# Performance work log

Hardware: AMD Instinct MI355X
Metric: run time of the kernel (lower is better)

## Reference

```python
import jax, jax.numpy as jnp
import numpy as np

N, S, C, K, V = 8, 8192, 1, 1024, 64  # batch, samples, n_channels, n_classes, vec_len


def setup_inputs() -> dict:
    key = jax.random.key(0)
    k1, k2 = jax.random.split(key)
    x0 = jax.random.normal(k1, (N, S, C, V), dtype=jnp.float32)
    embedding0 = jax.random.normal(k2, (C, K, V), dtype=jnp.float32) * 0.001
    return {"x0": x0, "embedding0": embedding0}


def reference(x0, embedding0):
    # normalize=False path of the original module
    x = x0
    emb = embedding0
    Ns = x.shape[0] * x.shape[1]
    xf = x.reshape(Ns, C, V)  # (Ns, C, V)
    # squared distances ||x - e||^2 without materializing (Ns, C, K, V)
    d2 = (
        jnp.sum(xf * xf, axis=-1)[:, :, None]
        - 2.0 * jnp.einsum("ncv,ckv->nck", xf, emb)
        + jnp.sum(emb * emb, axis=-1)[None, :, :]
    )
    index = jnp.argmin(d2, axis=2)  # (Ns, C); argmin of dist == argmin of dist^2
    # histogram entropy (matches torch histc over bins 0..K-1, divided by len(index)=Ns)
    counts = jnp.zeros((K,), jnp.float32).at[index.reshape(-1)].add(1.0)
    prob = counts / Ns
    safe_log = jnp.log(jnp.where(counts > 0, prob, 1.0))
    entropy = -jnp.sum(jnp.where(counts > 0, prob * safe_log, 0.0))
    # gather codewords: embedding[c, index[n,c]]
    output = emb[jnp.arange(C)[None, :], index].reshape(x.shape)
    out0 = jax.lax.stop_gradient(output - x) + x  # straight-through
    out1 = jnp.sum((jax.lax.stop_gradient(x) - output) ** 2, axis=-1)  # (N,S,C)
    out2 = jnp.sum((x - jax.lax.stop_gradient(output)) ** 2, axis=-1)  # (N,S,C)
    return (out0, out1, out2, entropy)
```

## Files before the change

### kernel.cpp

```cpp
#include <hip/hip_runtime.h>
#include <math.h>

#define NS   65536
#define KK   1024
#define VV   64
#define SPB  256
#define NB   (NS / SPB)
#define CBB  131072

#define OUT0_OFF 0
#define OUT1_OFF 4194304
#define OUT2_OFF 4259840
#define ENT_OFF  4325376


typedef __attribute__((ext_vector_type(8))) short bf16x8;
typedef __attribute__((ext_vector_type(4))) float f32x4;

#define ASYNC16(gp, lp) __builtin_amdgcn_global_load_lds(                      \
    (const __attribute__((address_space(1))) unsigned int*)(gp),               \
    (__attribute__((address_space(3))) unsigned int*)(lp), 16, 0, 0)

__device__ __forceinline__ short f2bf(float f) {
    unsigned u = __float_as_uint(f);
    u = (u + 0x7fffu + ((u >> 16) & 1u)) >> 16;
    return (short)u;
}

__global__ void vq_prep(const float* __restrict__ emb, unsigned int* __restrict__ hist,
                        float* __restrict__ cinit, short* __restrict__ cb,
                        unsigned int* __restrict__ entCnt) {
    int t = blockIdx.x * blockDim.x + threadIdx.x;
    if (t == 0) entCnt[0] = 0u;
    if (t < KK) {
        hist[t] = 0u;
        const float4* e4 = (const float4*)(emb + (size_t)t * VV);
        const int ch = t >> 8, cw = t & 255;
        short* base = cb + (size_t)ch * (256 * VV) + cw * 64;
        float s = 0.f;
        union { short sh[8]; bf16x8 v; } pk;
        #pragma unroll
        for (int g = 0; g < 8; ++g) {
            float4 f0 = e4[2 * g], f1 = e4[2 * g + 1];
            s = fmaf(f0.x, f0.x, s); s = fmaf(f0.y, f0.y, s);
            s = fmaf(f0.z, f0.z, s); s = fmaf(f0.w, f0.w, s);
            s = fmaf(f1.x, f1.x, s); s = fmaf(f1.y, f1.y, s);
            s = fmaf(f1.z, f1.z, s); s = fmaf(f1.w, f1.w, s);
            pk.sh[0] = f2bf(f0.x); pk.sh[1] = f2bf(f0.y);
            pk.sh[2] = f2bf(f0.z); pk.sh[3] = f2bf(f0.w);
            pk.sh[4] = f2bf(f1.x); pk.sh[5] = f2bf(f1.y);
            pk.sh[6] = f2bf(f1.z); pk.sh[7] = f2bf(f1.w);
            *(bf16x8*)(base + ((g ^ (cw & 7)) * 8)) = pk.v;
        }
        cinit[t] = 1.0f - 0.5f * s;
    }
}

__global__ __launch_bounds__(1024, 4) void vq_main(
    const float* __restrict__ x, const float* __restrict__ emb,
    const float* __restrict__ cinit, const short* __restrict__ cb,
    unsigned int* __restrict__ hist,
    float* __restrict__ out0, float* __restrict__ out1, float* __restrict__ out2,
    float* __restrict__ entOut)
{
    __shared__ __align__(16) char  sCB[CBB];
    __shared__ __align__(16) float sCI[KK];
    __shared__ unsigned sPk2[2][SPB];
    __shared__ float    sXn[SPB];
    __shared__ float    sPart[16];
    __shared__ unsigned sLast;

    const int tid  = threadIdx.x;
    const int lane = tid & 63;
    const int wv   = tid >> 6;
    const int grp  = wv & 7;
    const int kh   = wv >> 3;
    const int col  = lane & 15;
    const int quad = lane >> 4;
    const int samp0 = blockIdx.x * SPB;
    const int wbase = grp * 32;

    {
        const char* g0 = (const char*)cb;
        #pragma unroll
        for (int i = 0; i < 8; ++i) {
            const int off = (i * 1024 + tid) * 16;
            ASYNC16(g0 + off, sCB + off);
        }
        sCI[tid] = cinit[tid];
    }

    bf16x8 a[4];
    float  xn[2];
    #pragma unroll
    for (int mt = 0; mt < 2; ++mt) {
        const float* xp = x + (size_t)(samp0 + wbase + mt * 16 + col) * VV + quad * 8;
        float4 p0 = *(const float4*)(xp);
        float4 p1 = *(const float4*)(xp + 4);
        float4 p2 = *(const float4*)(xp + 32);
        float4 p3 = *(const float4*)(xp + 36);
        bf16x8 lo, hi;
        lo[0]=f2bf(p0.x); lo[1]=f2bf(p0.y); lo[2]=f2bf(p0.z); lo[3]=f2bf(p0.w);
        lo[4]=f2bf(p1.x); lo[5]=f2bf(p1.y); lo[6]=f2bf(p1.z); lo[7]=f2bf(p1.w);
        hi[0]=f2bf(p2.x); hi[1]=f2bf(p2.y); hi[2]=f2bf(p2.z); hi[3]=f2bf(p2.w);
        hi[4]=f2bf(p3.x); hi[5]=f2bf(p3.y); hi[6]=f2bf(p3.z); hi[7]=f2bf(p3.w);
        a[2 * mt] = lo; a[2 * mt + 1] = hi;
        float s = 0.f;
        s=fmaf(p0.x,p0.x,s); s=fmaf(p0.y,p0.y,s); s=fmaf(p0.z,p0.z,s); s=fmaf(p0.w,p0.w,s);
        s=fmaf(p1.x,p1.x,s); s=fmaf(p1.y,p1.y,s); s=fmaf(p1.z,p1.z,s); s=fmaf(p1.w,p1.w,s);
        s=fmaf(p2.x,p2.x,s); s=fmaf(p2.y,p2.y,s); s=fmaf(p2.z,p2.z,s); s=fmaf(p2.w,p2.w,s);
        s=fmaf(p3.x,p3.x,s); s=fmaf(p3.y,p3.y,s); s=fmaf(p3.z,p3.z,s); s=fmaf(p3.w,p3.w,s);
        xn[mt] = s;
    }
    if (kh == 0) {
        #pragma unroll
        for (int mt = 0; mt < 2; ++mt) {
            xn[mt] += __shfl_xor(xn[mt], 16, 64);
            xn[mt] += __shfl_xor(xn[mt], 32, 64);
        }
    }
    __syncthreads();

    unsigned pm[8];
    #pragma unroll
    for (int j = 0; j < 8; ++j) pm[j] = 0u;

    const int rb0off = col * 128 + ((quad ^ (col & 7)) << 4);
    const int rb1off = col * 128 + (((4 + quad) ^ (col & 7)) << 4);
    const unsigned invc = 1023u - (unsigned)(kh * 512) - (unsigned)col;
    const char*  B  = sCB + kh * 65536;
    const float* CI = sCI + kh * 512;

    unsigned pkp[8];
    #pragma unroll 8
    for (int t = 0; t < 32; ++t) {
        bf16x8 b0 = *(const bf16x8*)(B + t * 2048 + rb0off);
        bf16x8 b1 = *(const bf16x8*)(B + t * 2048 + rb1off);
        float ci = CI[t * 16 + col];
        f32x4 cv = {ci, ci, ci, ci};
        const unsigned inv = invc - (unsigned)(t * 16);
        unsigned pk2[8];
        #pragma unroll
        for (int mt = 0; mt < 2; ++mt) {
            f32x4 acc = __builtin_amdgcn_mfma_f32_16x16x32_bf16(a[2*mt],     b0, cv,  0, 0, 0);
            acc       = __builtin_amdgcn_mfma_f32_16x16x32_bf16(a[2*mt + 1], b1, acc, 0, 0, 0);
            #pragma unroll
            for (int r = 0; r < 4; ++r)
                pk2[mt*4+r] = (__float_as_uint(acc[r]) & 0xFFFFFC00u) | inv;
        }
        if (t & 1) {
            #pragma unroll
            for (int j = 0; j < 8; ++j) {
                unsigned t2 = pkp[j] > pk2[j] ? pkp[j] : pk2[j];
                pm[j] = pm[j] > t2 ? pm[j] : t2;
            }
        } else {
            #pragma unroll
            for (int j = 0; j < 8; ++j) pkp[j] = pk2[j];
        }
    }

    #pragma unroll
    for (int off = 1; off < 16; off <<= 1) {
        #pragma unroll
        for (int j = 0; j < 8; ++j) {
            unsigned o = (unsigned)__shfl_xor((int)pm[j], off, 64);
            pm[j] = (o > pm[j]) ? o : pm[j];
        }
    }
    if (col == 0) {
        #pragma unroll
        for (int mt = 0; mt < 2; ++mt)
            #pragma unroll
            for (int r = 0; r < 4; ++r)
                sPk2[kh][wbase + mt * 16 + quad * 4 + r] = pm[mt * 4 + r];
    }
    if (kh == 0 && quad == 0) {
        #pragma unroll
        for (int mt = 0; mt < 2; ++mt) sXn[wbase + mt * 16 + col] = xn[mt];
    }
    __syncthreads();

    if (tid < SPB) {
        unsigned pa = sPk2[0][tid], pb = sPk2[1][tid];
        unsigned p  = pa > pb ? pa : pb;
        sPk2[0][tid] = p;
        int   code = 1023 - (int)(p & 1023u);
        float sf   = __uint_as_float(p & 0xFFFFFC00u);
        float d    = fmaf(-2.f, sf - 1.0f, sXn[tid]);
        int n = samp0 + tid;
        out1[n] = d;
        out2[n] = d;
        atomicAdd(&hist[code], 1u);
    }
    __syncthreads();

    {
        float4* dstB = (float4*)(out0 + (size_t)samp0 * VV);
        #pragma unroll
        for (int i = 0; i < 4; ++i) {
            const int idx  = i * 1024 + tid;
            const int smp  = idx >> 4;
            const int part = idx & 15;
            const int code = 1023 - (int)(sPk2[0][smp] & 1023u);
            dstB[idx] = *((const float4*)(emb + (size_t)code * VV) + part);
        }
    }

    __syncthreads();
    unsigned int* entCnt = (unsigned int*)entOut;
    if (tid == 0)
        sLast = (__hip_atomic_fetch_add(entCnt, 1u, __ATOMIC_ACQ_REL,
                                        __HIP_MEMORY_SCOPE_AGENT) == (NB - 1)) ? 1u : 0u;
    __syncthreads();
    if (sLast) {
        unsigned c = __hip_atomic_load(&hist[tid], __ATOMIC_RELAXED,
                                       __HIP_MEMORY_SCOPE_AGENT);
        float e = 0.f;
        if (c) { float p = (float)c * (1.0f / (float)NS); e = -p * logf(p); }
        #pragma unroll
        for (int off = 32; off > 0; off >>= 1) e += __shfl_down(e, off, 64);
        if (lane == 0) sPart[wv] = e;
        __syncthreads();
        if (tid == 0) {
            float s = 0.f;
            #pragma unroll
            for (int i = 0; i < 16; ++i) s += sPart[i];
            entOut[0] = s;
        }
    }
}

extern "C" void kernel_launch(void* const* d_in, const int* in_sizes, int n_in,
                              void* d_out, int out_size, void* d_ws, size_t ws_size,
                              hipStream_t stream) {
    const float* x   = (const float*)d_in[0];
    const float* emb = (const float*)d_in[1];
    float* out = (float*)d_out;
    unsigned int* hist  = (unsigned int*)d_ws;
    float*        cinit = (float*)((char*)d_ws + 4096);
    short*        cb    = (short*)((char*)d_ws + 8192);

    vq_prep<<<4, 256, 0, stream>>>(emb, hist, cinit, cb, (unsigned int*)(out + ENT_OFF));
    vq_main<<<NB, 1024, 0, stream>>>(x, emb, cinit, cb, hist,
                                     out + OUT0_OFF, out + OUT1_OFF, out + OUT2_OFF,
                                     out + ENT_OFF);
}
```

Measured before the change: 111.3 us.

## Swap operand roles: stage samples in LDS, stream codebook from global into registers

```diff
diff --git a/kernel.cpp b/kernel.cpp
--- a/kernel.cpp
+++ b/kernel.cpp
@@ -4,9 +4,11 @@
 #define NS   65536
 #define KK   1024
 #define VV   64
-#define SPB  256
+#define SPB  128
 #define NB   (NS / SPB)
-#define CBB  131072
+#define NW   8
+#define TPW  4
+#define NPASS 2
 
 #define OUT0_OFF 0
 #define OUT1_OFF 4194304
@@ -16,10 +18,6 @@
 
 typedef __attribute__((ext_vector_type(8))) short bf16x8;
 typedef __attribute__((ext_vector_type(4))) float f32x4;
-
-#define ASYNC16(gp, lp) __builtin_amdgcn_global_load_lds(                      \
-    (const __attribute__((address_space(1))) unsigned int*)(gp),               \
-    (__attribute__((address_space(3))) unsigned int*)(lp), 16, 0, 0)
 
 __device__ __forceinline__ short f2bf(float f) {
     unsigned u = __float_as_uint(f);
@@ -35,8 +33,7 @@
     if (t < KK) {
         hist[t] = 0u;
         const float4* e4 = (const float4*)(emb + (size_t)t * VV);
-        const int ch = t >> 8, cw = t & 255;
-        short* base = cb + (size_t)ch * (256 * VV) + cw * 64;
+        const int T = t >> 4, cc = t & 15;
         float s = 0.f;
         union { short sh[8]; bf16x8 v; } pk;
         #pragma unroll
@@ -50,143 +47,128 @@
             pk.sh[2] = f2bf(f0.z); pk.sh[3] = f2bf(f0.w);
             pk.sh[4] = f2bf(f1.x); pk.sh[5] = f2bf(f1.y);
             pk.sh[6] = f2bf(f1.z); pk.sh[7] = f2bf(f1.w);
-            *(bf16x8*)(base + ((g ^ (cw & 7)) * 8)) = pk.v;
+            short* dst = cb + (size_t)T * 1024 + (g >> 2) * 512 + ((g & 3) * 16 + cc) * 8;
+            *(bf16x8*)dst = pk.v;
         }
         cinit[t] = 1.0f - 0.5f * s;
     }
 }
 
-__global__ __launch_bounds__(1024, 4) void vq_main(
+__global__ __launch_bounds__(512, 4) void vq_main(
     const float* __restrict__ x, const float* __restrict__ emb,
     const float* __restrict__ cinit, const short* __restrict__ cb,
     unsigned int* __restrict__ hist,
     float* __restrict__ out0, float* __restrict__ out1, float* __restrict__ out2,
     float* __restrict__ entOut)
 {
-    __shared__ __align__(16) char  sCB[CBB];
-    __shared__ __align__(16) float sCI[KK];
-    __shared__ unsigned sPk2[2][SPB];
+    __shared__ __align__(16) char  sA[SPB * 128];
     __shared__ float    sXn[SPB];
-    __shared__ float    sPart[16];
+    __shared__ unsigned sRed[SPB][NW + 1];
+    __shared__ unsigned sPkF[SPB];
+    __shared__ float    sPart[NW];
     __shared__ unsigned sLast;
 
     const int tid  = threadIdx.x;
     const int lane = tid & 63;
     const int wv   = tid >> 6;
-    const int grp  = wv & 7;
-    const int kh   = wv >> 3;
     const int col  = lane & 15;
     const int quad = lane >> 4;
     const int samp0 = blockIdx.x * SPB;
-    const int wbase = grp * 32;
 
     {
-        const char* g0 = (const char*)cb;
-        #pragma unroll
-        for (int i = 0; i < 8; ++i) {
-            const int off = (i * 1024 + tid) * 16;
-            ASYNC16(g0 + off, sCB + off);
-        }
-        sCI[tid] = cinit[tid];
-    }
-
-    bf16x8 a[4];
-    float  xn[2];
+        const int s = tid >> 2, q = tid & 3;
+        const float4* xp = (const float4*)(x + (size_t)(samp0 + s) * VV + q * 16);
+        float4 f0 = xp[0], f1 = xp[1], f2 = xp[2], f3 = xp[3];
+        float sm = 0.f;
+        sm=fmaf(f0.x,f0.x,sm); sm=fmaf(f0.y,f0.y,sm); sm=fmaf(f0.z,f0.z,sm); sm=fmaf(f0.w,f0.w,sm);
+        sm=fmaf(f1.x,f1.x,sm); sm=fmaf(f1.y,f1.y,sm); sm=fmaf(f1.z,f1.z,sm); sm=fmaf(f1.w,f1.w,sm);
+        sm=fmaf(f2.x,f2.x,sm); sm=fmaf(f2.y,f2.y,sm); sm=fmaf(f2.z,f2.z,sm); sm=fmaf(f2.w,f2.w,sm);
+        sm=fmaf(f3.x,f3.x,sm); sm=fmaf(f3.y,f3.y,sm); sm=fmaf(f3.z,f3.z,sm); sm=fmaf(f3.w,f3.w,sm);
+        union { short sh[8]; bf16x8 v; } pa, pb;
+        pa.sh[0]=f2bf(f0.x); pa.sh[1]=f2bf(f0.y); pa.sh[2]=f2bf(f0.z); pa.sh[3]=f2bf(f0.w);
+        pa.sh[4]=f2bf(f1.x); pa.sh[5]=f2bf(f1.y); pa.sh[6]=f2bf(f1.z); pa.sh[7]=f2bf(f1.w);
+        pb.sh[0]=f2bf(f2.x); pb.sh[1]=f2bf(f2.y); pb.sh[2]=f2bf(f2.z); pb.sh[3]=f2bf(f2.w);
+        pb.sh[4]=f2bf(f3.x); pb.sh[5]=f2bf(f3.y); pb.sh[6]=f2bf(f3.z); pb.sh[7]=f2bf(f3.w);
+        short* base = (short*)(sA + s * 128);
+        *(bf16x8*)(base + ((((2*q)    ) ^ (s & 7)) << 3)) = pa.v;
+        *(bf16x8*)(base + ((((2*q) + 1) ^ (s & 7)) << 3)) = pb.v;
+        sm += __shfl_xor(sm, 1, 64);
+        sm += __shfl_xor(sm, 2, 64);
+        if ((tid & 3) == 0) sXn[s] = sm;
+    }
+
+    const int rb0 = col * 128 + (( quad      ^ (col & 7)) << 4);
+    const int rb1 = col * 128 + (((4 + quad) ^ (col & 7)) << 4);
+
+    unsigned pmv[8];
     #pragma unroll
-    for (int mt = 0; mt < 2; ++mt) {
-        const float* xp = x + (size_t)(samp0 + wbase + mt * 16 + col) * VV + quad * 8;
-        float4 p0 = *(const float4*)(xp);
-        float4 p1 = *(const float4*)(xp + 4);
-        float4 p2 = *(const float4*)(xp + 32);
-        float4 p3 = *(const float4*)(xp + 36);
-        bf16x8 lo, hi;
-        lo[0]=f2bf(p0.x); lo[1]=f2bf(p0.y); lo[2]=f2bf(p0.z); lo[3]=f2bf(p0.w);
-        lo[4]=f2bf(p1.x); lo[5]=f2bf(p1.y); lo[6]=f2bf(p1.z); lo[7]=f2bf(p1.w);
-        hi[0]=f2bf(p2.x); hi[1]=f2bf(p2.y); hi[2]=f2bf(p2.z); hi[3]=f2bf(p2.w);
-        hi[4]=f2bf(p3.x); hi[5]=f2bf(p3.y); hi[6]=f2bf(p3.z); hi[7]=f2bf(p3.w);
-        a[2 * mt] = lo; a[2 * mt + 1] = hi;
-        float s = 0.f;
-        s=fmaf(p0.x,p0.x,s); s=fmaf(p0.y,p0.y,s); s=fmaf(p0.z,p0.z,s); s=fmaf(p0.w,p0.w,s);
-        s=fmaf(p1.x,p1.x,s); s=fmaf(p1.y,p1.y,s); s=fmaf(p1.z,p1.z,s); s=fmaf(p1.w,p1.w,s);
-        s=fmaf(p2.x,p2.x,s); s=fmaf(p2.y,p2.y,s); s=fmaf(p2.z,p2.z,s); s=fmaf(p2.w,p2.w,s);
-        s=fmaf(p3.x,p3.x,s); s=fmaf(p3.y,p3.y,s); s=fmaf(p3.z,p3.z,s); s=fmaf(p3.w,p3.w,s);
-        xn[mt] = s;
-    }
-    if (kh == 0) {
-        #pragma unroll
-        for (int mt = 0; mt < 2; ++mt) {
-            xn[mt] += __shfl_xor(xn[mt], 16, 64);
-            xn[mt] += __shfl_xor(xn[mt], 32, 64);
-        }
-    }
-    __syncthreads();
-
-    unsigned pm[8];
+    for (int j = 0; j < 8; ++j) pmv[j] = 0u;
+
+    for (int p = 0; p < NPASS; ++p) {
+        bf16x8   af0[TPW], af1[TPW];
+        f32x4    cv[TPW];
+        unsigned inv[TPW][4];
+        const int Tb = p * 32 + wv * TPW;
+        #pragma unroll
+        for (int t = 0; t < TPW; ++t) {
+            const char* cp = (const char*)cb + (size_t)(Tb + t) * 2048;
+            af0[t] = *(const bf16x8*)(cp + lane * 16);
+            af1[t] = *(const bf16x8*)(cp + 1024 + lane * 16);
+            cv[t]  = *(const f32x4*)(cinit + (Tb + t) * 16 + quad * 4);
+            const unsigned ib = 1023u - (unsigned)((Tb + t) * 16 + quad * 4);
+            inv[t][0] = ib; inv[t][1] = ib - 1; inv[t][2] = ib - 2; inv[t][3] = ib - 3;
+        }
+        if (p == 0) __syncthreads();
+
+        #pragma unroll
+        for (int mt = 0; mt < 8; ++mt) {
+            const char* Bp = sA + mt * 2048;
+            bf16x8 b0 = *(const bf16x8*)(Bp + rb0);
+            bf16x8 b1 = *(const bf16x8*)(Bp + rb1);
+            #pragma unroll
+            for (int t = 0; t < TPW; ++t) {
+                f32x4 acc = __builtin_amdgcn_mfma_f32_16x16x32_bf16(af0[t], b0, cv[t], 0, 0, 0);
+                acc       = __builtin_amdgcn_mfma_f32_16x16x32_bf16(af1[t], b1, acc,   0, 0, 0);
+                unsigned u0 = (__float_as_uint(acc[0]) & 0xFFFFFC00u) | inv[t][0];
+                unsigned u1 = (__float_as_uint(acc[1]) & 0xFFFFFC00u) | inv[t][1];
+                unsigned u2 = (__float_as_uint(acc[2]) & 0xFFFFFC00u) | inv[t][2];
+                unsigned u3 = (__float_as_uint(acc[3]) & 0xFFFFFC00u) | inv[t][3];
+                unsigned m0 = u0 > u1 ? u0 : u1;
+                unsigned m1 = u2 > u3 ? u2 : u3;
+                unsigned mm = m0 > m1 ? m0 : m1;
+                pmv[mt] = pmv[mt] > mm ? pmv[mt] : mm;
+            }
+        }
+    }
+
     #pragma unroll
-    for (int j = 0; j < 8; ++j) pm[j] = 0u;
-
-    const int rb0off = col * 128 + ((quad ^ (col & 7)) << 4);
-    const int rb1off = col * 128 + (((4 + quad) ^ (col & 7)) << 4);
-    const unsigned invc = 1023u - (unsigned)(kh * 512) - (unsigned)col;
-    const char*  B  = sCB + kh * 65536;
-    const float* CI = sCI + kh * 512;
-
-    unsigned pkp[8];
-    #pragma unroll 8
-    for (int t = 0; t < 32; ++t) {
-        bf16x8 b0 = *(const bf16x8*)(B + t * 2048 + rb0off);
-        bf16x8 b1 = *(const bf16x8*)(B + t * 2048 + rb1off);
-        float ci = CI[t * 16 + col];
-        f32x4 cv = {ci, ci, ci, ci};
-        const unsigned inv = invc - (unsigned)(t * 16);
-        unsigned pk2[8];
-        #pragma unroll
-        for (int mt = 0; mt < 2; ++mt) {
-            f32x4 acc = __builtin_amdgcn_mfma_f32_16x16x32_bf16(a[2*mt],     b0, cv,  0, 0, 0);
-            acc       = __builtin_amdgcn_mfma_f32_16x16x32_bf16(a[2*mt + 1], b1, acc, 0, 0, 0);
-            #pragma unroll
-            for (int r = 0; r < 4; ++r)
-                pk2[mt*4+r] = (__float_as_uint(acc[r]) & 0xFFFFFC00u) | inv;
-        }
-        if (t & 1) {
-            #pragma unroll
-            for (int j = 0; j < 8; ++j) {
-                unsigned t2 = pkp[j] > pk2[j] ? pkp[j] : pk2[j];
-                pm[j] = pm[j] > t2 ? pm[j] : t2;
-            }
-        } else {
-            #pragma unroll
-            for (int j = 0; j < 8; ++j) pkp[j] = pk2[j];
-        }
-    }
-
-    #pragma unroll
-    for (int off = 1; off < 16; off <<= 1) {
-        #pragma unroll
-        for (int j = 0; j < 8; ++j) {
-            unsigned o = (unsigned)__shfl_xor((int)pm[j], off, 64);
-            pm[j] = (o > pm[j]) ? o : pm[j];
-        }
-    }
-    if (col == 0) {
-        #pragma unroll
-        for (int mt = 0; mt < 2; ++mt)
-            #pragma unroll
-            for (int r = 0; r < 4; ++r)
-                sPk2[kh][wbase + mt * 16 + quad * 4 + r] = pm[mt * 4 + r];
-    }
-    if (kh == 0 && quad == 0) {
-        #pragma unroll
-        for (int mt = 0; mt < 2; ++mt) sXn[wbase + mt * 16 + col] = xn[mt];
+    for (int j = 0; j < 8; ++j) {
+        unsigned o;
+        o = (unsigned)__shfl_xor((int)pmv[j], 16, 64); pmv[j] = o > pmv[j] ? o : pmv[j];
+        o = (unsigned)__shfl_xor((int)pmv[j], 32, 64); pmv[j] = o > pmv[j] ? o : pmv[j];
+    }
+    {
+        unsigned w0 = (quad & 1) ? pmv[1] : pmv[0];
+        unsigned w1 = (quad & 1) ? pmv[3] : pmv[2];
+        unsigned lo = (quad & 2) ? w1 : w0;
+        unsigned w2 = (quad & 1) ? pmv[5] : pmv[4];
+        unsigned w3 = (quad & 1) ? pmv[7] : pmv[6];
+        unsigned hi = (quad & 2) ? w3 : w2;
+        sRed[quad * 16 + col][wv]       = lo;
+        sRed[(quad + 4) * 16 + col][wv] = hi;
     }
     __syncthreads();
 
     if (tid < SPB) {
-        unsigned pa = sPk2[0][tid], pb = sPk2[1][tid];
-        unsigned p  = pa > pb ? pa : pb;
-        sPk2[0][tid] = p;
-        int   code = 1023 - (int)(p & 1023u);
-        float sf   = __uint_as_float(p & 0xFFFFFC00u);
+        unsigned pbest = sRed[tid][0];
+        #pragma unroll
+        for (int w = 1; w < NW; ++w) {
+            unsigned o = sRed[tid][w];
+            pbest = o > pbest ? o : pbest;
+        }
+        sPkF[tid] = pbest;
+        int   code = 1023 - (int)(pbest & 1023u);
+        float sf   = __uint_as_float(pbest & 0xFFFFFC00u);
         float d    = fmaf(-2.f, sf - 1.0f, sXn[tid]);
         int n = samp0 + tid;
         out1[n] = d;
@@ -199,10 +181,10 @@
         float4* dstB = (float4*)(out0 + (size_t)samp0 * VV);
         #pragma unroll
         for (int i = 0; i < 4; ++i) {
-            const int idx  = i * 1024 + tid;
+            const int idx  = i * 512 + tid;
             const int smp  = idx >> 4;
             const int part = idx & 15;
-            const int code = 1023 - (int)(sPk2[0][smp] & 1023u);
+            const int code = 1023 - (int)(sPkF[smp] & 1023u);
             dstB[idx] = *((const float4*)(emb + (size_t)code * VV) + part);
         }
     }
@@ -214,10 +196,13 @@
                                         __HIP_MEMORY_SCOPE_AGENT) == (NB - 1)) ? 1u : 0u;
     __syncthreads();
     if (sLast) {
-        unsigned c = __hip_atomic_load(&hist[tid], __ATOMIC_RELAXED,
-                                       __HIP_MEMORY_SCOPE_AGENT);
         float e = 0.f;
-        if (c) { float p = (float)c * (1.0f / (float)NS); e = -p * logf(p); }
+        #pragma unroll
+        for (int i = 0; i < 2; ++i) {
+            unsigned c = __hip_atomic_load(&hist[i * 512 + tid], __ATOMIC_RELAXED,
+                                           __HIP_MEMORY_SCOPE_AGENT);
+            if (c) { float pr = (float)c * (1.0f / (float)NS); e -= pr * logf(pr); }
+        }
         #pragma unroll
         for (int off = 32; off > 0; off >>= 1) e += __shfl_down(e, off, 64);
         if (lane == 0) sPart[wv] = e;
@@ -225,7 +210,7 @@
         if (tid == 0) {
             float s = 0.f;
             #pragma unroll
-            for (int i = 0; i < 16; ++i) s += sPart[i];
+            for (int i = 0; i < NW; ++i) s += sPart[i];
             entOut[0] = s;
         }
     }
@@ -242,7 +227,7 @@
     short*        cb    = (short*)((char*)d_ws + 8192);
 
     vq_prep<<<4, 256, 0, stream>>>(emb, hist, cinit, cb, (unsigned int*)(out + ENT_OFF));
-    vq_main<<<NB, 1024, 0, stream>>>(x, emb, cinit, cb, hist,
-                                     out + OUT0_OFF, out + OUT1_OFF, out + OUT2_OFF,
-                                     out + ENT_OFF);
-}
+    vq_main<<<NB, 512, 0, stream>>>(x, emb, cinit, cb, hist,
+                                    out + OUT0_OFF, out + OUT1_OFF, out + OUT2_OFF,
+                                    out + ENT_OFF);
+}
```

After: 106.7 us. -4.1%, faster.
